# Optimization experiments

Measured on AMD Instinct MI355X. Metric: run time of the kernel, lower is better.

The kernel has to match this reference:

```python
import jax, jax.numpy as jnp
import numpy as np

N, C, H = 384, 128, 4

def setup_inputs() -> dict:
    key = jax.random.key(0)
    ks = jax.random.split(key, 8)
    s = 1.0 / np.sqrt(C).astype(np.float32)
    pair = jax.random.normal(ks[0], (N, N, C), jnp.float32)
    mask = (jax.random.uniform(ks[1], (N, N)) > 0.5).astype(jnp.float32)
    return {
        'pair': pair,
        'mask': mask,
        'ln_w': jnp.ones((C,), jnp.float32),
        'ln_b': jnp.zeros((C,), jnp.float32),
        'bias_w': jax.random.normal(ks[2], (H, C), jnp.float32) * s,
        'q_w': jax.random.normal(ks[3], (C, C), jnp.float32) * s,
        'k_w': jax.random.normal(ks[4], (C, C), jnp.float32) * s,
        'v_w': jax.random.normal(ks[5], (C, C), jnp.float32) * s,
        'g_w': jax.random.normal(ks[6], (C, C), jnp.float32) * s,
        'o_w': jax.random.normal(ks[7], (C, C), jnp.float32) * s,
    }

def reference(pair, mask, ln_w, ln_b, bias_w, q_w, k_w, v_w, g_w, o_w):
    n, _, c = pair.shape
    h = bias_w.shape[0]
    d = c // h  # qkv_dim = c_pair // num_head
    # LayerNorm over channel dim (eps=1e-5, torch default)
    mu = jnp.mean(pair, axis=-1, keepdims=True)
    var = jnp.var(pair, axis=-1, keepdims=True)
    x = (pair - mu) * jax.lax.rsqrt(var + 1e-5) * ln_w + ln_b  # [N,N,C]
    # nonbatched pair bias: Linear(C->H), then permute(2,0,1) -> [H,N,N]
    bias = jnp.einsum('ijc,hc->hij', x, bias_w)
    # per-row (b) attention over keys j; Linear weight W: y = x @ W.T
    q = (x @ q_w.T).reshape(n, n, h, d)
    k = (x @ k_w.T).reshape(n, n, h, d)
    v = (x @ v_w.T).reshape(n, n, h, d)
    mask_bias = 1e9 * (mask - 1.0)  # [N,N]: -inf-like where masked per row b, key j
    logits = jnp.einsum('bihd,bjhd->bhij', q, k) * (1.0 / np.sqrt(d).astype(np.float32))
    logits = logits + bias[None, :, :, :] + mask_bias[:, None, None, :]
    w = jax.nn.softmax(logits, axis=-1)  # [N,H,N,N]
    o = jnp.einsum('bhij,bjhd->bihd', w, v).reshape(n, n, c)
    gate = jax.nn.sigmoid(x @ g_w.T)
    return (gate * o) @ o_w.T  # [N,N,C]
```

## Files before the change

### kernel.cpp

```cpp
#include <hip/hip_runtime.h>
#include <hip/hip_bf16.h>

#define NN 384
#define CC 128
#define HH 4
#define DD 32
#define QK_SCALE 0.17677669529663687f

typedef float f32x4 __attribute__((ext_vector_type(4)));
typedef short s16x8 __attribute__((ext_vector_type(8)));
typedef short s16x4 __attribute__((ext_vector_type(4)));
typedef unsigned short u16;
typedef unsigned int u32;

__device__ __forceinline__ u16 f2b(float f) {
  union { float f; u32 u; } c; c.f = f;
  u32 u = c.u + 0x7FFFu + ((c.u >> 16) & 1u);
  return (u16)(u >> 16);
}
__device__ __forceinline__ u32 pack2(float a, float b) {
  return (u32)f2b(a) | ((u32)f2b(b) << 16);
}
__device__ __forceinline__ float b2f_lo(u32 u) {
  union { u32 u; float f; } c; c.u = u << 16; return c.f;
}
__device__ __forceinline__ float b2f_hi(u32 u) {
  union { u32 u; float f; } c; c.u = u & 0xFFFF0000u; return c.f;
}
__device__ __forceinline__ s16x4 mk4(u32 a, u32 b) {
  union { u32 u[2]; s16x4 v; } c; c.u[0] = a; c.u[1] = b; return c.v;
}

#define MFMA32(a, b, c) __builtin_amdgcn_mfma_f32_16x16x32_bf16((a), (b), (c), 0, 0, 0)
#define MFMA16(a, b, c) __builtin_amdgcn_mfma_f32_16x16x16bf16_1k((a), (b), (c), 0, 0, 0)

__global__ __launch_bounds__(256) void k_ln_bias(
    const float* __restrict__ pair, const float* __restrict__ ln_w,
    const float* __restrict__ ln_b, const float* __restrict__ bias_w,
    const float* __restrict__ q_w, const float* __restrict__ k_w,
    const float* __restrict__ v_w, const float* __restrict__ g_w,
    const float* __restrict__ o_w, u16* __restrict__ xb,
    u16* __restrict__ biasb, u16* __restrict__ wqk, u16* __restrict__ wv,
    u16* __restrict__ wg, u16* __restrict__ wo) {
  if (blockIdx.x == 36864) {
    const int t = threadIdx.x;
    const float2* q2 = (const float2*)q_w;
    const float2* k2 = (const float2*)k_w;
    const float2* v2 = (const float2*)v_w;
    const float2* g2 = (const float2*)g_w;
    const float2* o2 = (const float2*)o_w;
    u32* dq = (u32*)wqk;
    u32* dk = (u32*)wqk + 8192;
    u32* dv = (u32*)wv;
    u32* dg = (u32*)wg;
    u32* dw = (u32*)wo;
    for (int i = t; i < 8192; i += 256) {
      float2 a = q2[i];
      dq[i] = pack2(a.x * QK_SCALE, a.y * QK_SCALE);
      a = k2[i]; dk[i] = pack2(a.x, a.y);
      a = v2[i]; dv[i] = pack2(a.x, a.y);
      a = g2[i]; dg[i] = pack2(a.x, a.y);
      a = o2[i]; dw[i] = pack2(a.x, a.y);
    }
    return;
  }
  const int wave = threadIdx.x >> 6;
  const int l = threadIdx.x & 63;
  const int p = blockIdx.x * 4 + wave;

  const float2 v = ((const float2*)pair)[(size_t)p * 64 + l];
  float s = v.x + v.y, sq = v.x * v.x + v.y * v.y;
#pragma unroll
  for (int off = 32; off >= 1; off >>= 1) {
    s += __shfl_xor(s, off);
    sq += __shfl_xor(sq, off);
  }
  const float mean = s * (1.0f / 128.0f);
  const float rstd = rsqrtf(sq * (1.0f / 128.0f) - mean * mean + 1e-5f);
  const float2 lw = ((const float2*)ln_w)[l];
  const float2 lb2 = ((const float2*)ln_b)[l];
  const float x0 = (v.x - mean) * rstd * lw.x + lb2.x;
  const float x1 = (v.y - mean) * rstd * lw.y + lb2.y;
  ((u32*)xb)[(size_t)p * 64 + l] = pack2(x0, x1);

#pragma unroll
  for (int h = 0; h < HH; ++h) {
    const float2 bw = ((const float2*)bias_w)[h * 64 + l];
    float bp = x0 * bw.x + x1 * bw.y;
#pragma unroll
    for (int off = 32; off >= 1; off >>= 1) bp += __shfl_xor(bp, off);
    if (l == 0) biasb[(size_t)h * NN * NN + p] = f2b(bp);
  }
}

__global__ __launch_bounds__(256, 4) void k_qkv(
    const u16* __restrict__ xb, const u16* __restrict__ wqk,
    const u16* __restrict__ wv, u16* __restrict__ qg, u16* __restrict__ kg,
    u16* __restrict__ vtg) {
  const int bid = blockIdx.x;
  const int b = bid / 6, jt = bid % 6;
  const int jrow0 = b * NN + jt * 64;
  const int jloc0 = jt * 64;
  const int t = threadIdx.x, w = t >> 6, l = t & 63;
  const int lr = l & 15, lg = l >> 4;

  {
    const int n0 = w * 64;
    f32x4 acc[4][4];
#pragma unroll
    for (int ns = 0; ns < 4; ++ns)
#pragma unroll
      for (int ms = 0; ms < 4; ++ms) acc[ns][ms] = (f32x4){0.f, 0.f, 0.f, 0.f};
#pragma unroll
    for (int cs = 0; cs < 8; ++cs) {
      s16x4 bx[4];
#pragma unroll
      for (int ms = 0; ms < 4; ++ms)
        bx[ms] = *(const s16x4*)&xb[(size_t)(jrow0 + ms * 16 + lr) * CC +
                                    cs * 16 + lg * 4];
#pragma unroll
      for (int ns = 0; ns < 4; ++ns) {
        const s16x4 aW =
            *(const s16x4*)&wqk[(n0 + ns * 16 + lr) * CC + cs * 16 + lg * 4];
#pragma unroll
        for (int ms = 0; ms < 4; ++ms)
          acc[ns][ms] = MFMA16(aW, bx[ms], acc[ns][ms]);
      }
    }
    u16* base = (n0 >= 128) ? kg : qg;
#pragma unroll
    for (int ns = 0; ns < 4; ++ns) {
      const int n = n0 + ns * 16 + lg * 4;
      const int h = (n >> 5) & 3, d = n & 31;
#pragma unroll
      for (int ms = 0; ms < 4; ++ms) {
        u32* dst = (u32*)(base + (size_t)(b * 4 + h) * 12288 +
                          (jloc0 + ms * 16 + lr) * 32 + d);
        dst[0] = pack2(acc[ns][ms][0], acc[ns][ms][1]);
        dst[1] = pack2(acc[ns][ms][2], acc[ns][ms][3]);
      }
    }
  }

  {
    const int m0 = (w & 1) * 32, n0v = (w >> 1) * 64;
    f32x4 accv[2][4];
#pragma unroll
    for (int ms = 0; ms < 2; ++ms)
#pragma unroll
      for (int ns = 0; ns < 4; ++ns) accv[ms][ns] = (f32x4){0.f, 0.f, 0.f, 0.f};
#pragma unroll
    for (int cs = 0; cs < 4; ++cs) {
      s16x8 ax[2], bw[4];
#pragma unroll
      for (int ms = 0; ms < 2; ++ms)
        ax[ms] = *(const s16x8*)&xb[(size_t)(jrow0 + m0 + ms * 16 + lr) * CC +
                                    cs * 32 + lg * 8];
#pragma unroll
      for (int ns = 0; ns < 4; ++ns)
        bw[ns] =
            *(const s16x8*)&wv[(n0v + ns * 16 + lr) * CC + cs * 32 + lg * 8];
#pragma unroll
      for (int ms = 0; ms < 2; ++ms)
#pragma unroll
        for (int ns = 0; ns < 4; ++ns)
          accv[ms][ns] = MFMA32(ax[ms], bw[ns], accv[ms][ns]);
    }
#pragma unroll
    for (int ms = 0; ms < 2; ++ms) {
#pragma unroll
      for (int ns = 0; ns < 4; ++ns) {
        const int n = n0v + ns * 16 + lr;
        const int h = n >> 5, d = n & 31;
        const int j = jloc0 + m0 + ms * 16 + lg * 4;
        u32* dst = (u32*)(vtg + (size_t)(b * 4 + h) * 12288 + d * NN + j);
        dst[0] = pack2(accv[ms][ns][0], accv[ms][ns][1]);
        dst[1] = pack2(accv[ms][ns][2], accv[ms][ns][3]);
      }
    }
  }
}

__global__ __launch_bounds__(256, 3) void k_attn(
    const u16* __restrict__ qg, const u16* __restrict__ kg,
    const u16* __restrict__ vtg, const u16* __restrict__ biasb,
    const float* __restrict__ mask, float* __restrict__ io) {
  __shared__ float mb[NN];
  const int bid = blockIdx.x;
  const int bh = bid >> 1, half = bid & 1;
  const int b = bh >> 2, h = bh & 3;
  const int t = threadIdx.x, w = t >> 6, l = t & 63;
  const int lr = l & 15, lg = l >> 4;

  for (int i = t; i < NN; i += 256) mb[i] = 1e9f * (mask[b * NN + i] - 1.0f);
  __syncthreads();

  const int q0 = half * 192 + w * 48;
  const u16* qb = qg + (size_t)bh * 12288;
  const u16* kb = kg + (size_t)bh * 12288;
  const u16* vb = vtg + (size_t)bh * 12288;
  const u16* bb = biasb + (size_t)h * NN * NN;

  s16x8 bQ[3];
#pragma unroll
  for (int ms = 0; ms < 3; ++ms)
    bQ[ms] = *(const s16x8*)&qb[(q0 + ms * 16 + lr) * 32 + lg * 8];

  float mr[3], ls[3];
  f32x4 oa[3][2];
#pragma unroll
  for (int ms = 0; ms < 3; ++ms) {
    mr[ms] = -3.0e38f;
    ls[ms] = 0.f;
    oa[ms][0] = (f32x4){0.f, 0.f, 0.f, 0.f};
    oa[ms][1] = (f32x4){0.f, 0.f, 0.f, 0.f};
  }
  const f32x4 z4 = {0.f, 0.f, 0.f, 0.f};

  for (int kt = 0; kt < 6; ++kt) {
    s16x8 aK[4];
#pragma unroll
    for (int js = 0; js < 4; ++js)
      aK[js] = *(const s16x8*)&kb[(kt * 64 + js * 16 + lr) * 32 + lg * 8];

    f32x4 sT[3][4];
#pragma unroll
    for (int ms = 0; ms < 3; ++ms)
#pragma unroll
      for (int js = 0; js < 4; ++js) sT[ms][js] = MFMA32(aK[js], bQ[ms], z4);

#pragma unroll
    for (int js = 0; js < 4; ++js) {
      const int jb = kt * 64 + js * 16 + lg * 4;
      const f32x4 m4 = *(const f32x4*)&mb[jb];
#pragma unroll
      for (int ms = 0; ms < 3; ++ms) {
        const u32* bp = (const u32*)&bb[(size_t)(q0 + ms * 16 + lr) * NN + jb];
        const u32 b0 = bp[0], b1 = bp[1];
        sT[ms][js][0] += b2f_lo(b0) + m4[0];
        sT[ms][js][1] += b2f_hi(b0) + m4[1];
        sT[ms][js][2] += b2f_lo(b1) + m4[2];
        sT[ms][js][3] += b2f_hi(b1) + m4[3];
      }
    }

    u32 pk[3][4][2];
#pragma unroll
    for (int ms = 0; ms < 3; ++ms) {
      float tm = -3.0e38f;
#pragma unroll
      for (int js = 0; js < 4; ++js)
#pragma unroll
        for (int r = 0; r < 4; ++r) tm = fmaxf(tm, sT[ms][js][r]);
      tm = fmaxf(tm, __shfl_xor(tm, 16));
      tm = fmaxf(tm, __shfl_xor(tm, 32));
      const float nm = fmaxf(mr[ms], tm);
      const float sc = __expf(mr[ms] - nm);
      mr[ms] = nm;
      float ts = 0.f;
#pragma unroll
      for (int js = 0; js < 4; ++js)
#pragma unroll
        for (int r = 0; r < 4; ++r) {
          const float p = __expf(sT[ms][js][r] - nm);
          sT[ms][js][r] = p;
          ts += p;
        }
      ts += __shfl_xor(ts, 16);
      ts += __shfl_xor(ts, 32);
      ls[ms] = ls[ms] * sc + ts;
      oa[ms][0] *= sc;
      oa[ms][1] *= sc;
#pragma unroll
      for (int js = 0; js < 4; ++js) {
        pk[ms][js][0] = pack2(sT[ms][js][0], sT[ms][js][1]);
        pk[ms][js][1] = pack2(sT[ms][js][2], sT[ms][js][3]);
      }
    }

#pragma unroll
    for (int st = 0; st < 4; ++st) {
      const int jb = kt * 64 + st * 16 + lg * 4;
      s16x4 aV[2];
#pragma unroll
      for (int ns = 0; ns < 2; ++ns)
        aV[ns] = *(const s16x4*)&vb[(ns * 16 + lr) * NN + jb];
#pragma unroll
      for (int ms = 0; ms < 3; ++ms) {
        const s16x4 pb = mk4(pk[ms][st][0], pk[ms][st][1]);
#pragma unroll
        for (int ns = 0; ns < 2; ++ns)
          oa[ms][ns] = MFMA16(aV[ns], pb, oa[ms][ns]);
      }
    }
  }

#pragma unroll
  for (int ms = 0; ms < 3; ++ms) {
    const float inv = 1.0f / ls[ms];
    float* orow = io + ((size_t)b * NN + q0 + ms * 16 + lr) * CC + h * DD;
#pragma unroll
    for (int ns = 0; ns < 2; ++ns) {
      f32x4 vo = oa[ms][ns];
      vo *= inv;
      *(f32x4*)&orow[ns * 16 + lg * 4] = vo;
    }
  }
}

__global__ __launch_bounds__(256, 4) void k_gate_out(
    const u16* __restrict__ xb, const u16* __restrict__ wg,
    const u16* __restrict__ wo, float* __restrict__ io) {
  const int bid = blockIdx.x;
  const int t = threadIdx.x, w = t >> 6, l = t & 63;
  const int lr = l & 15, lg = l >> 4;
  const int m0g = bid * 64 + w * 16;

  f32x4 a1[8];
#pragma unroll
  for (int ns = 0; ns < 8; ++ns) a1[ns] = (f32x4){0.f, 0.f, 0.f, 0.f};
#pragma unroll
  for (int cs = 0; cs < 8; ++cs) {
    const s16x4 bx =
        *(const s16x4*)&xb[(size_t)(m0g + lr) * CC + cs * 16 + lg * 4];
#pragma unroll
    for (int ns = 0; ns < 8; ++ns) {
      const s16x4 aW =
          *(const s16x4*)&wg[(ns * 16 + lr) * CC + cs * 16 + lg * 4];
      a1[ns] = MFMA16(aW, bx, a1[ns]);
    }
  }

  s16x4 pk2[8];
#pragma unroll
  for (int ns = 0; ns < 8; ++ns) {
    const int gc = ns * 16 + lg * 4;
    const f32x4 ov = *(const f32x4*)&io[(size_t)(m0g + lr) * CC + gc];
    float av[4];
#pragma unroll
    for (int r = 0; r < 4; ++r)
      av[r] = ov[r] / (1.0f + __expf(-a1[ns][r]));
    pk2[ns] = mk4(pack2(av[0], av[1]), pack2(av[2], av[3]));
  }

  f32x4 a2[8];
#pragma unroll
  for (int ns = 0; ns < 8; ++ns) a2[ns] = (f32x4){0.f, 0.f, 0.f, 0.f};
#pragma unroll
  for (int cs = 0; cs < 8; ++cs) {
#pragma unroll
    for (int ns = 0; ns < 8; ++ns) {
      const s16x4 aW =
          *(const s16x4*)&wo[(ns * 16 + lr) * CC + cs * 16 + lg * 4];
      a2[ns] = MFMA16(aW, pk2[cs], a2[ns]);
    }
  }
#pragma unroll
  for (int ns = 0; ns < 8; ++ns)
    *(f32x4*)&io[(size_t)(m0g + lr) * CC + ns * 16 + lg * 4] = a2[ns];
}

extern "C" void kernel_launch(void* const* d_in, const int* in_sizes, int n_in,
                              void* d_out, int out_size, void* d_ws,
                              size_t ws_size, hipStream_t stream) {
  const float* pair = (const float*)d_in[0];
  const float* mask = (const float*)d_in[1];
  const float* ln_w = (const float*)d_in[2];
  const float* ln_b = (const float*)d_in[3];
  const float* bias_w = (const float*)d_in[4];
  const float* q_w = (const float*)d_in[5];
  const float* k_w = (const float*)d_in[6];
  const float* v_w = (const float*)d_in[7];
  const float* g_w = (const float*)d_in[8];
  const float* o_w = (const float*)d_in[9];

  char* wsb = (char*)d_ws;
  u16* xb = (u16*)wsb;
  u16* biasb = (u16*)(wsb + 37748736);
  u16* wqk = (u16*)(wsb + 38928384);
  u16* wv = (u16*)(wsb + 38993920);
  u16* wg = (u16*)(wsb + 39026688);
  u16* wo = (u16*)(wsb + 39059456);
  u16* qg = (u16*)(wsb + 39092224);
  u16* kg = (u16*)(wsb + 76840960);
  u16* vtg = (u16*)(wsb + 114589696);
  float* io = (float*)d_out;

  hipLaunchKernelGGL(k_ln_bias, dim3(NN * NN / 4 + 1), dim3(256), 0, stream,
                     pair, ln_w, ln_b, bias_w, q_w, k_w, v_w, g_w, o_w, xb,
                     biasb, wqk, wv, wg, wo);
  hipLaunchKernelGGL(k_qkv, dim3(NN * 6), dim3(256), 0, stream, xb, wqk, wv,
                     qg, kg, vtg);
  hipLaunchKernelGGL(k_attn, dim3(NN * HH * 2), dim3(256), 0, stream, qg, kg,
                     vtg, biasb, mask, io);
  hipLaunchKernelGGL(k_gate_out, dim3(NN * NN / 64), dim3(256), 0, stream, xb,
                     g_w ? wg : wg, wo, io);
}
```

Baseline: 664.9 us.

## Store bias and V in MFMA fragment layout, fuse QKV loops, widen MFMA

```diff
diff --git a/kernel.cpp b/kernel.cpp
--- a/kernel.cpp
+++ b/kernel.cpp
@@ -4,7 +4,6 @@
 #define NN 384
 #define CC 128
 #define HH 4
-#define DD 32
 #define QK_SCALE 0.17677669529663687f
 
 typedef float f32x4 __attribute__((ext_vector_type(4)));
@@ -20,6 +19,10 @@
 }
 __device__ __forceinline__ u32 pack2(float a, float b) {
   return (u32)f2b(a) | ((u32)f2b(b) << 16);
+}
+__device__ __forceinline__ u32 pack2t(float a, float b) {
+  union { float f; u32 u; } x, y; x.f = a; y.f = b;
+  return (x.u >> 16) | (y.u & 0xFFFF0000u);
 }
 __device__ __forceinline__ float b2f_lo(u32 u) {
   union { u32 u; float f; } c; c.u = u << 16; return c.f;
@@ -40,7 +43,7 @@
     const float* __restrict__ q_w, const float* __restrict__ k_w,
     const float* __restrict__ v_w, const float* __restrict__ g_w,
     const float* __restrict__ o_w, u16* __restrict__ xb,
-    u16* __restrict__ biasb, u16* __restrict__ wqk, u16* __restrict__ wv,
+    u16* __restrict__ biasf, u16* __restrict__ wqk, u16* __restrict__ wv,
     u16* __restrict__ wg, u16* __restrict__ wo) {
   if (blockIdx.x == 36864) {
     const int t = threadIdx.x;
@@ -83,107 +86,103 @@
   const float x1 = (v.y - mean) * rstd * lw.y + lb2.y;
   ((u32*)xb)[(size_t)p * 64 + l] = pack2(x0, x1);
 
+  const int i = p / NN;
+  const int j = p - i * NN;
+  const int slot = ((j & 12) << 4) + ((i & 15) << 2) + (j & 3);
 #pragma unroll
   for (int h = 0; h < HH; ++h) {
     const float2 bw = ((const float2*)bias_w)[h * 64 + l];
     float bp = x0 * bw.x + x1 * bw.y;
 #pragma unroll
     for (int off = 32; off >= 1; off >>= 1) bp += __shfl_xor(bp, off);
-    if (l == 0) biasb[(size_t)h * NN * NN + p] = f2b(bp);
-  }
-}
-
-__global__ __launch_bounds__(256, 4) void k_qkv(
+    if (l == 0)
+      biasf[(((h * 24 + (j >> 4)) * 24 + (i >> 4)) << 8) + slot] = f2b(bp);
+  }
+}
+
+__global__ __launch_bounds__(256) void k_qkv(
     const u16* __restrict__ xb, const u16* __restrict__ wqk,
     const u16* __restrict__ wv, u16* __restrict__ qg, u16* __restrict__ kg,
-    u16* __restrict__ vtg) {
+    u16* __restrict__ vtf) {
   const int bid = blockIdx.x;
-  const int b = bid / 6, jt = bid % 6;
-  const int jrow0 = b * NN + jt * 64;
-  const int jloc0 = jt * 64;
+  const int b = bid / 6, jt6 = bid % 6;
+  const int jrow0 = b * NN + jt6 * 64, jloc0 = jt6 * 64;
   const int t = threadIdx.x, w = t >> 6, l = t & 63;
   const int lr = l & 15, lg = l >> 4;
+  const int n0 = w * 64;
+  const int m0v = (w & 1) * 2;
+  const int n0v = (w >> 1) * 64;
+
+  f32x4 acc[4][4];
+  f32x4 accv[2][4];
+#pragma unroll
+  for (int a = 0; a < 4; ++a)
+#pragma unroll
+    for (int c = 0; c < 4; ++c) acc[a][c] = (f32x4){0.f, 0.f, 0.f, 0.f};
+#pragma unroll
+  for (int a = 0; a < 2; ++a)
+#pragma unroll
+    for (int c = 0; c < 4; ++c) accv[a][c] = (f32x4){0.f, 0.f, 0.f, 0.f};
+
+#pragma unroll
+  for (int cs = 0; cs < 4; ++cs) {
+    s16x8 bx[4];
+#pragma unroll
+    for (int ms = 0; ms < 4; ++ms)
+      bx[ms] = *(const s16x8*)&xb[(size_t)(jrow0 + ms * 16 + lr) * CC +
+                                  cs * 32 + lg * 8];
+#pragma unroll
+    for (int ns = 0; ns < 4; ++ns) {
+      const s16x8 aW =
+          *(const s16x8*)&wqk[(n0 + ns * 16 + lr) * CC + cs * 32 + lg * 8];
+#pragma unroll
+      for (int ms = 0; ms < 4; ++ms)
+        acc[ns][ms] = MFMA32(aW, bx[ms], acc[ns][ms]);
+      const s16x8 bV =
+          *(const s16x8*)&wv[(n0v + ns * 16 + lr) * CC + cs * 32 + lg * 8];
+#pragma unroll
+      for (int mv = 0; mv < 2; ++mv)
+        accv[mv][ns] = MFMA32(bx[m0v + mv], bV, accv[mv][ns]);
+    }
+  }
 
   {
-    const int n0 = w * 64;
-    f32x4 acc[4][4];
-#pragma unroll
-    for (int ns = 0; ns < 4; ++ns)
-#pragma unroll
-      for (int ms = 0; ms < 4; ++ms) acc[ns][ms] = (f32x4){0.f, 0.f, 0.f, 0.f};
-#pragma unroll
-    for (int cs = 0; cs < 8; ++cs) {
-      s16x4 bx[4];
-#pragma unroll
-      for (int ms = 0; ms < 4; ++ms)
-        bx[ms] = *(const s16x4*)&xb[(size_t)(jrow0 + ms * 16 + lr) * CC +
-                                    cs * 16 + lg * 4];
-#pragma unroll
-      for (int ns = 0; ns < 4; ++ns) {
-        const s16x4 aW =
-            *(const s16x4*)&wqk[(n0 + ns * 16 + lr) * CC + cs * 16 + lg * 4];
-#pragma unroll
-        for (int ms = 0; ms < 4; ++ms)
-          acc[ns][ms] = MFMA16(aW, bx[ms], acc[ns][ms]);
-      }
-    }
     u16* base = (n0 >= 128) ? kg : qg;
+    const int nb = n0 & 64;
 #pragma unroll
     for (int ns = 0; ns < 4; ++ns) {
-      const int n = n0 + ns * 16 + lg * 4;
-      const int h = (n >> 5) & 3, d = n & 31;
+      const int nl = nb + ns * 16 + lg * 4;
+      const int h = nl >> 5, d0 = nl & 31;
 #pragma unroll
       for (int ms = 0; ms < 4; ++ms) {
         u32* dst = (u32*)(base + (size_t)(b * 4 + h) * 12288 +
-                          (jloc0 + ms * 16 + lr) * 32 + d);
+                          (jloc0 + ms * 16 + lr) * 32 + d0);
         dst[0] = pack2(acc[ns][ms][0], acc[ns][ms][1]);
         dst[1] = pack2(acc[ns][ms][2], acc[ns][ms][3]);
       }
     }
   }
 
-  {
-    const int m0 = (w & 1) * 32, n0v = (w >> 1) * 64;
-    f32x4 accv[2][4];
-#pragma unroll
-    for (int ms = 0; ms < 2; ++ms)
-#pragma unroll
-      for (int ns = 0; ns < 4; ++ns) accv[ms][ns] = (f32x4){0.f, 0.f, 0.f, 0.f};
-#pragma unroll
-    for (int cs = 0; cs < 4; ++cs) {
-      s16x8 ax[2], bw[4];
-#pragma unroll
-      for (int ms = 0; ms < 2; ++ms)
-        ax[ms] = *(const s16x8*)&xb[(size_t)(jrow0 + m0 + ms * 16 + lr) * CC +
-                                    cs * 32 + lg * 8];
-#pragma unroll
-      for (int ns = 0; ns < 4; ++ns)
-        bw[ns] =
-            *(const s16x8*)&wv[(n0v + ns * 16 + lr) * CC + cs * 32 + lg * 8];
-#pragma unroll
-      for (int ms = 0; ms < 2; ++ms)
-#pragma unroll
-        for (int ns = 0; ns < 4; ++ns)
-          accv[ms][ns] = MFMA32(ax[ms], bw[ns], accv[ms][ns]);
-    }
-#pragma unroll
-    for (int ms = 0; ms < 2; ++ms) {
-#pragma unroll
-      for (int ns = 0; ns < 4; ++ns) {
-        const int n = n0v + ns * 16 + lr;
-        const int h = n >> 5, d = n & 31;
-        const int j = jloc0 + m0 + ms * 16 + lg * 4;
-        u32* dst = (u32*)(vtg + (size_t)(b * 4 + h) * 12288 + d * NN + j);
-        dst[0] = pack2(accv[ms][ns][0], accv[ms][ns][1]);
-        dst[1] = pack2(accv[ms][ns][2], accv[ms][ns][3]);
-      }
-    }
-  }
-}
-
-__global__ __launch_bounds__(256, 3) void k_attn(
+#pragma unroll
+  for (int mv = 0; mv < 2; ++mv) {
+#pragma unroll
+    for (int ns = 0; ns < 4; ++ns) {
+      const int n = n0v + ns * 16 + lr;
+      const int h = n >> 5;
+      const int dt = (n >> 4) & 1;
+      const int j0 = jloc0 + (m0v + mv) * 16;
+      u32* dst = (u32*)vtf +
+                 ((((size_t)(b * 4 + h)) * 24 + (j0 >> 4)) * 2 + dt) * 128 +
+                 l * 2;
+      dst[0] = pack2(accv[mv][ns][0], accv[mv][ns][1]);
+      dst[1] = pack2(accv[mv][ns][2], accv[mv][ns][3]);
+    }
+  }
+}
+
+__global__ __launch_bounds__(256) void k_attn(
     const u16* __restrict__ qg, const u16* __restrict__ kg,
-    const u16* __restrict__ vtg, const u16* __restrict__ biasb,
+    const u16* __restrict__ vtf, const u16* __restrict__ biasf,
     const float* __restrict__ mask, float* __restrict__ io) {
   __shared__ float mb[NN];
   const int bid = blockIdx.x;
@@ -195,11 +194,11 @@
   for (int i = t; i < NN; i += 256) mb[i] = 1e9f * (mask[b * NN + i] - 1.0f);
   __syncthreads();
 
-  const int q0 = half * 192 + w * 48;
+  const int q0 = half * 192 + w * 48, it0 = q0 >> 4;
   const u16* qb = qg + (size_t)bh * 12288;
   const u16* kb = kg + (size_t)bh * 12288;
-  const u16* vb = vtg + (size_t)bh * 12288;
-  const u16* bb = biasb + (size_t)h * NN * NN;
+  const u32* vt = (const u32*)vtf + (size_t)bh * 6144;
+  const u32* bbf = (const u32*)biasf + (size_t)h * 73728;
 
   s16x8 bQ[3];
 #pragma unroll
@@ -217,11 +216,28 @@
   }
   const f32x4 z4 = {0.f, 0.f, 0.f, 0.f};
 
+#pragma unroll
   for (int kt = 0; kt < 6; ++kt) {
     s16x8 aK[4];
 #pragma unroll
     for (int js = 0; js < 4; ++js)
       aK[js] = *(const s16x8*)&kb[(kt * 64 + js * 16 + lr) * 32 + lg * 8];
+    u32 bw[3][4][2];
+#pragma unroll
+    for (int ms = 0; ms < 3; ++ms)
+#pragma unroll
+      for (int js = 0; js < 4; ++js) {
+        const u32* p = bbf + ((kt * 4 + js) * 24 + it0 + ms) * 128 + l * 2;
+        bw[ms][js][0] = p[0];
+        bw[ms][js][1] = p[1];
+      }
+    s16x4 aV[4][2];
+#pragma unroll
+    for (int st = 0; st < 4; ++st)
+#pragma unroll
+      for (int ns = 0; ns < 2; ++ns)
+        aV[st][ns] =
+            *(const s16x4*)(vt + ((kt * 4 + st) * 2 + ns) * 128 + l * 2);
 
     f32x4 sT[3][4];
 #pragma unroll
@@ -235,8 +251,7 @@
       const f32x4 m4 = *(const f32x4*)&mb[jb];
 #pragma unroll
       for (int ms = 0; ms < 3; ++ms) {
-        const u32* bp = (const u32*)&bb[(size_t)(q0 + ms * 16 + lr) * NN + jb];
-        const u32 b0 = bp[0], b1 = bp[1];
+        const u32 b0 = bw[ms][js][0], b1 = bw[ms][js][1];
         sT[ms][js][0] += b2f_lo(b0) + m4[0];
         sT[ms][js][1] += b2f_hi(b0) + m4[1];
         sT[ms][js][2] += b2f_lo(b1) + m4[2];
@@ -273,24 +288,19 @@
       oa[ms][1] *= sc;
 #pragma unroll
       for (int js = 0; js < 4; ++js) {
-        pk[ms][js][0] = pack2(sT[ms][js][0], sT[ms][js][1]);
-        pk[ms][js][1] = pack2(sT[ms][js][2], sT[ms][js][3]);
+        pk[ms][js][0] = pack2t(sT[ms][js][0], sT[ms][js][1]);
+        pk[ms][js][1] = pack2t(sT[ms][js][2], sT[ms][js][3]);
       }
     }
 
 #pragma unroll
     for (int st = 0; st < 4; ++st) {
-      const int jb = kt * 64 + st * 16 + lg * 4;
-      s16x4 aV[2];
-#pragma unroll
-      for (int ns = 0; ns < 2; ++ns)
-        aV[ns] = *(const s16x4*)&vb[(ns * 16 + lr) * NN + jb];
 #pragma unroll
       for (int ms = 0; ms < 3; ++ms) {
         const s16x4 pb = mk4(pk[ms][st][0], pk[ms][st][1]);
 #pragma unroll
         for (int ns = 0; ns < 2; ++ns)
-          oa[ms][ns] = MFMA16(aV[ns], pb, oa[ms][ns]);
+          oa[ms][ns] = MFMA16(aV[st][ns], pb, oa[ms][ns]);
       }
     }
   }
@@ -298,7 +308,7 @@
 #pragma unroll
   for (int ms = 0; ms < 3; ++ms) {
     const float inv = 1.0f / ls[ms];
-    float* orow = io + ((size_t)b * NN + q0 + ms * 16 + lr) * CC + h * DD;
+    float* orow = io + ((size_t)b * NN + q0 + ms * 16 + lr) * CC + h * 32;
 #pragma unroll
     for (int ns = 0; ns < 2; ++ns) {
       f32x4 vo = oa[ms][ns];
@@ -308,7 +318,7 @@
   }
 }
 
-__global__ __launch_bounds__(256, 4) void k_gate_out(
+__global__ __launch_bounds__(256) void k_gate_out(
     const u16* __restrict__ xb, const u16* __restrict__ wg,
     const u16* __restrict__ wo, float* __restrict__ io) {
   const int bid = blockIdx.x;
@@ -320,22 +330,22 @@
 #pragma unroll
   for (int ns = 0; ns < 8; ++ns) a1[ns] = (f32x4){0.f, 0.f, 0.f, 0.f};
 #pragma unroll
-  for (int cs = 0; cs < 8; ++cs) {
-    const s16x4 bx =
-        *(const s16x4*)&xb[(size_t)(m0g + lr) * CC + cs * 16 + lg * 4];
+  for (int cs = 0; cs < 4; ++cs) {
+    const s16x8 bx =
+        *(const s16x8*)&xb[(size_t)(m0g + lr) * CC + cs * 32 + lg * 8];
 #pragma unroll
     for (int ns = 0; ns < 8; ++ns) {
-      const s16x4 aW =
-          *(const s16x4*)&wg[(ns * 16 + lr) * CC + cs * 16 + lg * 4];
-      a1[ns] = MFMA16(aW, bx, a1[ns]);
+      const s16x8 aW =
+          *(const s16x8*)&wg[(ns * 16 + lr) * CC + cs * 32 + lg * 8];
+      a1[ns] = MFMA32(aW, bx, a1[ns]);
     }
   }
 
   s16x4 pk2[8];
 #pragma unroll
   for (int ns = 0; ns < 8; ++ns) {
-    const int gc = ns * 16 + lg * 4;
-    const f32x4 ov = *(const f32x4*)&io[(size_t)(m0g + lr) * CC + gc];
+    const f32x4 ov =
+        *(const f32x4*)&io[(size_t)(m0g + lr) * CC + ns * 16 + lg * 4];
     float av[4];
 #pragma unroll
     for (int r = 0; r < 4; ++r)
@@ -350,9 +360,9 @@
   for (int cs = 0; cs < 8; ++cs) {
 #pragma unroll
     for (int ns = 0; ns < 8; ++ns) {
-      const s16x4 aW =
+      const s16x4 aW2 =
           *(const s16x4*)&wo[(ns * 16 + lr) * CC + cs * 16 + lg * 4];
-      a2[ns] = MFMA16(aW, pk2[cs], a2[ns]);
+      a2[ns] = MFMA16(aW2, pk2[cs], a2[ns]);
     }
   }
 #pragma unroll
@@ -376,23 +386,23 @@
 
   char* wsb = (char*)d_ws;
   u16* xb = (u16*)wsb;
-  u16* biasb = (u16*)(wsb + 37748736);
+  u16* biasf = (u16*)(wsb + 37748736);
   u16* wqk = (u16*)(wsb + 38928384);
   u16* wv = (u16*)(wsb + 38993920);
   u16* wg = (u16*)(wsb + 39026688);
   u16* wo = (u16*)(wsb + 39059456);
   u16* qg = (u16*)(wsb + 39092224);
   u16* kg = (u16*)(wsb + 76840960);
-  u16* vtg = (u16*)(wsb + 114589696);
+  u16* vtf = (u16*)(wsb + 114589696);
   float* io = (float*)d_out;
 
   hipLaunchKernelGGL(k_ln_bias, dim3(NN * NN / 4 + 1), dim3(256), 0, stream,
                      pair, ln_w, ln_b, bias_w, q_w, k_w, v_w, g_w, o_w, xb,
-                     biasb, wqk, wv, wg, wo);
+                     biasf, wqk, wv, wg, wo);
   hipLaunchKernelGGL(k_qkv, dim3(NN * 6), dim3(256), 0, stream, xb, wqk, wv,
-                     qg, kg, vtg);
+                     qg, kg, vtf);
   hipLaunchKernelGGL(k_attn, dim3(NN * HH * 2), dim3(256), 0, stream, qg, kg,
-                     vtg, biasb, mask, io);
+                     vtf, biasf, mask, io);
   hipLaunchKernelGGL(k_gate_out, dim3(NN * NN / 64), dim3(256), 0, stream, xb,
-                     g_w ? wg : wg, wo, io);
-}
+                     wg, wo, io);
+}
```

Result: faster. 620.5 us (-6.7%).
